# Optimization experiments

Hardware: AMD Instinct MI355X
Metric: run time of the kernel (lower is better)

Reference implementation:

```python
import jax, jax.numpy as jnp
import numpy as np

B, C, H, W = 4, 256, 64, 64
G = 32          # GroupNorm groups
EPS = 1e-6


def setup_inputs() -> dict:
    key = jax.random.key(0)
    ks = jax.random.split(key, 6)
    inp = {
        "x": jax.random.normal(ks[0], (B, C, H, W), dtype=jnp.float32),
        "gamma": jnp.ones((C,), jnp.float32),
        "beta": jnp.zeros((C,), jnp.float32),
        "wq": jax.random.normal(ks[1], (C, C), jnp.float32) * 0.02,
        "bq": jnp.zeros((C,), jnp.float32),
        "wk": jax.random.normal(ks[2], (C, C), jnp.float32) * 0.02,
        "bk": jnp.zeros((C,), jnp.float32),
        "wv": jax.random.normal(ks[3], (C, C), jnp.float32) * 0.02,
        "bv": jnp.zeros((C,), jnp.float32),
        "wp": jax.random.normal(ks[4], (C, C), jnp.float32) * 0.02,
        "bp": jnp.zeros((C,), jnp.float32),
    }
    return inp


def _group_norm(x, gamma, beta):
    b, c, h, w = x.shape
    xs = x.reshape(b, G, c // G, h, w)
    mu = xs.mean(axis=(2, 3, 4), keepdims=True)
    var = xs.var(axis=(2, 3, 4), keepdims=True)  # biased, matches torch GroupNorm
    xn = ((xs - mu) * jax.lax.rsqrt(var + EPS)).reshape(b, c, h, w)
    return xn * gamma[None, :, None, None] + beta[None, :, None, None]


def _conv1x1(s, w, bias):
    # 1x1 conv == per-pixel channel matmul
    return jnp.einsum('oc,bchw->bohw', w, s) + bias[None, :, None, None]


def reference(x, gamma, beta, wq, bq, wk, bk, wv, bv, wp, bp):
    b, c, h, w = x.shape
    s = _group_norm(x, gamma, beta)
    q = _conv1x1(s, wq, bq).reshape(b, c, h * w)  # [B, C, N]
    k = _conv1x1(s, wk, bk).reshape(b, c, h * w)
    v = _conv1x1(s, wv, bv).reshape(b, c, h * w)
    # scores[b,i,j] = sum_c q[b,c,i] k[b,c,j], scaled by C^-1/2
    scores = jnp.einsum('bci,bcj->bij', q, k) * (c ** -0.5)
    attn = jax.nn.softmax(scores, axis=2)
    # h_[b,c,i] = sum_j v[b,c,j] attn[b,i,j]
    h_ = jnp.einsum('bij,bcj->bci', attn, v).reshape(b, c, h, w)
    h_ = _conv1x1(h_, wp, bp)
    return x + h_
```

## Files before the change

### kernel.cpp

```cpp
#include <hip/hip_runtime.h>

#define BB 4
#define CCH 256
#define NPIX 4096
#define EPS 1e-6f

typedef __attribute__((ext_vector_type(8))) short bf16x8;
typedef __attribute__((ext_vector_type(4))) float f32x4;
typedef __attribute__((ext_vector_type(16))) float f32x16;

__device__ __forceinline__ unsigned short f2bf(float f) {
    return (unsigned short)((__float_as_uint(f) + 0x8000u) >> 16);
}
__device__ __forceinline__ float bf2f(unsigned short h) {
    return __uint_as_float((unsigned)h << 16);
}
__device__ __forceinline__ void gl2lds16(const void* g, void* l) {
    __builtin_amdgcn_global_load_lds(
        (const __attribute__((address_space(1))) unsigned int*)g,
        (__attribute__((address_space(3))) unsigned int*)l, 16, 0, 0);
}

__global__ __launch_bounds__(256) void gn_stats(
    const float* __restrict__ x, float2* __restrict__ pst,
    const float* __restrict__ wq, const float* __restrict__ wk,
    const float* __restrict__ wv, const float* __restrict__ wp,
    unsigned short* __restrict__ wb) {
    int bid = blockIdx.x;
    int t = threadIdx.x;
    if (bid >= 256) {
        int e = (bid - 256) * 256 + t;
        const float* srcs[4] = {wp, wq, wk, wv};
#pragma unroll
        for (int m = 0; m < 4; ++m) {
            float4 v = ((const float4*)srcs[m])[e];
            ushort4 hh;
            hh.x = f2bf(v.x); hh.y = f2bf(v.y);
            hh.z = f2bf(v.z); hh.w = f2bf(v.w);
            *(ushort4*)(wb + (size_t)m * 65536 + (size_t)e * 4) = hh;
        }
        return;
    }
    int b = bid >> 6, g = (bid >> 1) & 31, h = bid & 1;
    const float4* x4 = (const float4*)(x + (size_t)(b * CCH + g * 8) * NPIX);
    float s = 0.f, ss = 0.f;
    for (int e = h * 4096 + t; e < h * 4096 + 4096; e += 256) {
        float4 v = x4[e];
        s += v.x + v.y + v.z + v.w;
        ss += v.x * v.x + v.y * v.y + v.z * v.z + v.w * v.w;
    }
    __shared__ float rs[256], rss[256];
    rs[t] = s; rss[t] = ss;
    __syncthreads();
    for (int off = 128; off > 0; off >>= 1) {
        if (t < (unsigned)off) {
            rs[t] += rs[t + off];
            rss[t] += rss[t + off];
        }
        __syncthreads();
    }
    if (t == 0) pst[bid] = make_float2(rs[0], rss[0]);
}

__global__ __launch_bounds__(256) void gn_norm(
    const float* __restrict__ x, const float2* __restrict__ pst,
    const float* __restrict__ gamma, const float* __restrict__ beta,
    unsigned short* __restrict__ sb) {
    int bid = blockIdx.x;
    int b = bid >> 6, g = (bid >> 1) & 31, h = bid & 1;
    float2 p0 = pst[bid & ~1];
    float2 p1 = pst[bid | 1];
    const float inv = 1.0f / (float)(8 * NPIX);
    float m = (p0.x + p1.x) * inv;
    float var = (p0.y + p1.y) * inv - m * m;
    float rstd = rsqrtf(var + EPS);
    float scale[8], shift[8];
#pragma unroll
    for (int ci = 0; ci < 8; ++ci) {
        float ga = gamma[g * 8 + ci], be = beta[g * 8 + ci];
        scale[ci] = rstd * ga;
        shift[ci] = be - m * scale[ci];
    }
    const float4* x4 = (const float4*)(x + (size_t)(b * CCH + g * 8) * NPIX);
#pragma unroll 1
    for (int r = 0; r < 2; ++r) {
        int pq = h * 512 + r * 256 + threadIdx.x;
        __align__(16) unsigned short hh[4][8];
#pragma unroll
        for (int ci = 0; ci < 8; ++ci) {
            float4 v = x4[ci * 1024 + pq];
            hh[0][ci] = f2bf(v.x * scale[ci] + shift[ci]);
            hh[1][ci] = f2bf(v.y * scale[ci] + shift[ci]);
            hh[2][ci] = f2bf(v.z * scale[ci] + shift[ci]);
            hh[3][ci] = f2bf(v.w * scale[ci] + shift[ci]);
        }
        size_t base = ((size_t)(b * NPIX + pq * 4) << 8) + g * 8;
#pragma unroll
        for (int p = 0; p < 4; ++p)
            *(uint4*)(sb + base + (size_t)p * 256) = *(const uint4*)hh[p];
    }
}

__global__ __launch_bounds__(256) void qkv_mfma(
    const unsigned short* __restrict__ sb, const unsigned short* __restrict__ wb,
    const float* __restrict__ bq, const float* __restrict__ bk,
    const float* __restrict__ bv,
    unsigned short* __restrict__ qT, unsigned short* __restrict__ kT,
    unsigned short* __restrict__ vB) {
    __shared__ __align__(16) char lds[34816];
    const int tid = threadIdx.x, lane = tid & 63, w = tid >> 6;
    const int ln15 = lane & 15, q = lane >> 4;
    const int n0 = blockIdx.x * 128;
    const int co0 = blockIdx.y * 128;
    const int z = blockIdx.z;
    const unsigned short* wm = wb + (size_t)(z + 1) * 65536;
    const float* bias = (z == 0) ? bq : (z == 1) ? bk : bv;

    f32x4 acc[2][8];
#pragma unroll
    for (int i2 = 0; i2 < 2; ++i2)
#pragma unroll
        for (int nf = 0; nf < 8; ++nf) {
            acc[i2][nf][0] = 0.f; acc[i2][nf][1] = 0.f;
            acc[i2][nf][2] = 0.f; acc[i2][nf][3] = 0.f;
        }

#pragma unroll 1
    for (int kt = 0; kt < 4; ++kt) {
#pragma unroll
        for (int r = 0; r < 4; ++r) {
            int gch = r * 256 + tid;
            int row = gch >> 3, sidx = gch & 7;
            int cc = sidx ^ (row & 7);
            gl2lds16(sb + ((size_t)(n0 + row) << 8) + kt * 64 + cc * 8,
                     &lds[r * 4096 + w * 1024]);
            gl2lds16(wm + ((size_t)(co0 + row) << 8) + kt * 64 + cc * 8,
                     &lds[16384 + r * 4096 + w * 1024]);
        }
        __syncthreads();
#pragma unroll
        for (int kk = 0; kk < 2; ++kk) {
            int kc = kk * 4 + q;
            bf16x8 af[2], bf[8];
#pragma unroll
            for (int i2 = 0; i2 < 2; ++i2) {
                int row = w * 32 + i2 * 16 + ln15;
                af[i2] = *(const bf16x8*)&lds[row * 128 + ((kc ^ (row & 7)) << 4)];
            }
#pragma unroll
            for (int nf = 0; nf < 8; ++nf) {
                int row = nf * 16 + ln15;
                bf[nf] = *(const bf16x8*)&lds[16384 + row * 128 + ((kc ^ (row & 7)) << 4)];
            }
#pragma unroll
            for (int i2 = 0; i2 < 2; ++i2)
#pragma unroll
                for (int nf = 0; nf < 8; ++nf)
                    acc[i2][nf] = __builtin_amdgcn_mfma_f32_16x16x32_bf16(
                        af[i2], bf[nf], acc[i2][nf], 0, 0, 0);
        }
        __syncthreads();
    }

    float bias_l[8];
#pragma unroll
    for (int nf = 0; nf < 8; ++nf) bias_l[nf] = bias[co0 + nf * 16 + ln15];
    const float scl = (z == 0) ? 0.0625f : 1.0f;
    unsigned short* T = (unsigned short*)lds;
    if (z < 2) {
#pragma unroll
        for (int i2 = 0; i2 < 2; ++i2)
#pragma unroll
            for (int nf = 0; nf < 8; ++nf)
#pragma unroll
                for (int r = 0; r < 4; ++r) {
                    int n_l = w * 32 + i2 * 16 + q * 4 + r;
                    int co_l = nf * 16 + ln15;
                    T[n_l * 136 + co_l] = f2bf((acc[i2][nf][r] + bias_l[nf]) * scl);
                }
    } else {
#pragma unroll
        for (int i2 = 0; i2 < 2; ++i2)
#pragma unroll
            for (int nf = 0; nf < 8; ++nf)
#pragma unroll
                for (int r = 0; r < 4; ++r) {
                    int n_l = w * 32 + i2 * 16 + q * 4 + r;
                    int co_l = nf * 16 + ln15;
                    T[co_l * 136 + n_l] = f2bf(acc[i2][nf][r] + bias_l[nf]);
                }
    }
    __syncthreads();
    int row = tid >> 1, half = tid & 1;
    const uint4* src = (const uint4*)&T[row * 136 + half * 64];
    uint4* dst;
    if (z < 2) {
        unsigned short* qk = (z == 0) ? qT : kT;
        dst = (uint4*)(qk + ((size_t)(n0 + row) << 8) + co0 + half * 64);
    } else {
        int b2 = n0 >> 12, pix0 = n0 & 4095;
        dst = (uint4*)(vB + ((size_t)(b2 * CCH + co0 + row) << 12) + pix0 + half * 64);
    }
#pragma unroll
    for (int u = 0; u < 8; ++u) dst[u] = src[u];
}

__global__ __launch_bounds__(512, 1) void attn_mfma(
    const unsigned short* __restrict__ qT, const unsigned short* __restrict__ kT,
    const unsigned short* __restrict__ vB,
    unsigned short* __restrict__ pO, float* __restrict__ pml) {
    __shared__ __align__(16) char lds[147456];
    const int tid = threadIdx.x, lane = tid & 63, w = tid >> 6;
    const int l31 = lane & 31, lh = lane >> 5;
    const int bx = blockIdx.x;
    const int xk = bx & 7;
    const int b = xk >> 1, bjh = xk & 1;
    const int itile = bx >> 3;
    const int i0 = itile * 128;
    const int jbase = bjh * 2048;
    const size_t nb = (size_t)b * NPIX;
    const int iqb = (w >> 1) * 32;
    const int jh = w & 1, jwb = jh * 32;
    const int ipb = (w & 1) * 64;
    const int cqb = (w >> 1) * 64;

#pragma unroll
    for (int t = 0; t < 8; ++t) {
        int gch = (w * 8 + t) * 64 + lane;
        int row = gch >> 5, sc = gch & 31;
        int cc = sc ^ (row & 7);
        gl2lds16(qT + ((nb + i0 + row) << 8) + cc * 8, &lds[(w * 8 + t) * 1024]);
    }
    __syncthreads();
    bf16x8 qf[16];
    {
        int row = iqb + l31;
#pragma unroll
        for (int kc = 0; kc < 16; ++kc) {
            int sc = kc * 2 + lh;
            qf[kc] = *(const bf16x8*)&lds[row * 512 + ((sc ^ (row & 7)) << 4)];
        }
    }
    __syncthreads();

    f32x16 O[2][2];
#pragma unroll
    for (int ig = 0; ig < 2; ++ig)
#pragma unroll
        for (int cg = 0; cg < 2; ++cg)
#pragma unroll
            for (int r = 0; r < 16; ++r) O[ig][cg][r] = 0.f;
    float l_acc[16];
#pragma unroll
    for (int r = 0; r < 16; ++r) l_acc[r] = 0.f;

    {
        const int j0 = jbase;
#pragma unroll
        for (int t = 0; t < 4; ++t) {
            int gch = (w * 4 + t) * 64 + lane;
            int row = gch >> 5, sc = gch & 31;
            int cc = sc ^ (row & 7);
            gl2lds16(kT + ((nb + j0 + row) << 8) + cc * 8, &lds[(w * 4 + t) * 1024]);
        }
#pragma unroll
        for (int t = 0; t < 4; ++t) {
            int gch = (w * 4 + t) * 64 + lane;
            int c = gch >> 3, sv = gch & 7;
            int jc = sv ^ (c & 7);
            gl2lds16(vB + ((size_t)(b * CCH + c) << 12) + j0 + jc * 8,
                     &lds[65536 + (w * 4 + t) * 1024]);
        }
    }

#pragma unroll 1
    for (int jt = 0; jt < 32; ++jt) {
        const int kb_ = (jt & 1) * 32768;
        const int vb_ = 65536 + (jt & 1) * 32768;
        const int kbn = ((jt + 1) & 1) * 32768;
        const int vbn = 65536 + ((jt + 1) & 1) * 32768;

        asm volatile("s_waitcnt vmcnt(4)" ::: "memory");
        __builtin_amdgcn_s_barrier();

        f32x16 S0, S1;
#pragma unroll
        for (int r = 0; r < 16; ++r) { S0[r] = 0.f; S1[r] = 0.f; }
        __builtin_amdgcn_s_setprio(1);
        {
            int krow = jwb + l31;
            int ksw = kb_ + krow * 512;
#pragma unroll
            for (int kc = 0; kc < 8; ++kc) {
                int sc0 = (2 * kc) * 2 + lh;
                int sc1 = (2 * kc + 1) * 2 + lh;
                bf16x8 k0 = *(const bf16x8*)&lds[ksw + ((sc0 ^ (krow & 7)) << 4)];
                bf16x8 k1 = *(const bf16x8*)&lds[ksw + ((sc1 ^ (krow & 7)) << 4)];
                S0 = __builtin_amdgcn_mfma_f32_32x32x16_bf16(qf[2 * kc], k0, S0, 0, 0, 0);
                S1 = __builtin_amdgcn_mfma_f32_32x32x16_bf16(qf[2 * kc + 1], k1, S1, 0, 0, 0);
            }
        }
        __builtin_amdgcn_s_setprio(0);

        {
            int col = jwb + l31;
            int chs = (col >> 3) << 4;
            int cof = (col & 7) << 1;
#pragma unroll
            for (int r = 0; r < 16; ++r) {
                float p = __expf(S0[r] + S1[r]);
                l_acc[r] += p;
                int row = iqb + (r & 3) + 8 * (r >> 2) + 4 * lh;
                *(unsigned short*)&lds[131072 + row * 128 +
                    (chs ^ ((row & 7) << 4)) + cof] = f2bf(p);
            }
        }
        asm volatile("s_waitcnt lgkmcnt(0)" ::: "memory");
        __builtin_amdgcn_sched_barrier(0);
        asm volatile("s_waitcnt vmcnt(0)" ::: "memory");
        __builtin_amdgcn_s_barrier();

        if (jt < 31) {
            const int j0n = jbase + (jt + 1) * 64;
#pragma unroll
            for (int t = 0; t < 4; ++t) {
                int gch = (w * 4 + t) * 64 + lane;
                int row = gch >> 5, sc = gch & 31;
                int cc = sc ^ (row & 7);
                gl2lds16(kT + ((nb + j0n + row) << 8) + cc * 8,
                         &lds[kbn + (w * 4 + t) * 1024]);
            }
        }

        __builtin_amdgcn_s_setprio(1);
        {
            int pr0 = ipb + l31, pr1 = ipb + 32 + l31;
            int vc0 = cqb + l31, vc1 = cqb + 32 + l31;
#pragma unroll
            for (int kc = 0; kc < 4; ++kc) {
                int pc = kc * 2 + lh;
                bf16x8 pf0 = *(const bf16x8*)&lds[131072 + pr0 * 128 + ((pc ^ (pr0 & 7)) << 4)];
                bf16x8 pf1 = *(const bf16x8*)&lds[131072 + pr1 * 128 + ((pc ^ (pr1 & 7)) << 4)];
                bf16x8 vf0 = *(const bf16x8*)&lds[vb_ + vc0 * 128 + ((pc ^ (vc0 & 7)) << 4)];
                bf16x8 vf1 = *(const bf16x8*)&lds[vb_ + vc1 * 128 + ((pc ^ (vc1 & 7)) << 4)];
                O[0][0] = __builtin_amdgcn_mfma_f32_32x32x16_bf16(pf0, vf0, O[0][0], 0, 0, 0);
                O[0][1] = __builtin_amdgcn_mfma_f32_32x32x16_bf16(pf0, vf1, O[0][1], 0, 0, 0);
                O[1][0] = __builtin_amdgcn_mfma_f32_32x32x16_bf16(pf1, vf0, O[1][0], 0, 0, 0);
                O[1][1] = __builtin_amdgcn_mfma_f32_32x32x16_bf16(pf1, vf1, O[1][1], 0, 0, 0);
            }
        }
        __builtin_amdgcn_s_setprio(0);

        if (jt < 31) {
            const int j0n = jbase + (jt + 1) * 64;
#pragma unroll
            for (int t = 0; t < 4; ++t) {
                int gch = (w * 4 + t) * 64 + lane;
                int c = gch >> 3, sv = gch & 7;
                int jc = sv ^ (c & 7);
                gl2lds16(vB + ((size_t)(b * CCH + c) << 12) + j0n + jc * 8,
                         &lds[vbn + (w * 4 + t) * 1024]);
            }
        }
    }

    size_t pbase = (size_t)bx * (128 * 256);
#pragma unroll
    for (int ig = 0; ig < 2; ++ig)
#pragma unroll
        for (int cg = 0; cg < 2; ++cg)
#pragma unroll
            for (int r = 0; r < 16; ++r) {
                int i = ipb + ig * 32 + (r & 3) + 8 * (r >> 2) + 4 * lh;
                int c = cqb + cg * 32 + l31;
                pO[pbase + i * 256 + c] = f2bf(O[ig][cg][r]);
            }
#pragma unroll
    for (int r = 0; r < 16; ++r) {
        float l = l_acc[r];
        l += __shfl_xor(l, 1);
        l += __shfl_xor(l, 2);
        l += __shfl_xor(l, 4);
        l += __shfl_xor(l, 8);
        l += __shfl_xor(l, 16);
        if (l31 == 0) {
            int row = iqb + (r & 3) + 8 * (r >> 2) + 4 * lh;
            pml[bx * 256 + jh * 128 + row] = l;
        }
    }
}

__global__ __launch_bounds__(256) void attn_merge(
    const unsigned short* __restrict__ pO, const float* __restrict__ pml,
    unsigned short* __restrict__ hN) {
    int bid = blockIdx.x;
    int b = bid & 3, itile = (bid >> 2) & 31, ih = (bid >> 7) & 1;
    int base = itile * 8 + b * 2;
    __shared__ float fs[64];
    int t = threadIdx.x;
    if (t < 64) {
        float l = 0.f;
#pragma unroll
        for (int s = 0; s < 2; ++s) {
            int px = (base + s) * 256 + ih * 64 + t;
            l += pml[px] + pml[px + 128];
        }
        fs[t] = 1.0f / l;
    }
    __syncthreads();
    int i = t >> 2, cq = t & 3;
    float f = fs[i];
    int row = ih * 64 + i;
    size_t nrow = ((size_t)(b * NPIX + itile * 128 + row)) << 8;
#pragma unroll
    for (int p = 0; p < 16; ++p) {
        int c = p * 16 + cq * 4;
        float o0 = 0.f, o1 = 0.f, o2 = 0.f, o3 = 0.f;
#pragma unroll
        for (int s = 0; s < 2; ++s) {
            ushort4 a = *(const ushort4*)&pO[(size_t)(base + s) * 32768 + row * 256 + c];
            o0 += bf2f(a.x); o1 += bf2f(a.y); o2 += bf2f(a.z); o3 += bf2f(a.w);
        }
        ushort4 h;
        h.x = f2bf(o0 * f); h.y = f2bf(o1 * f);
        h.z = f2bf(o2 * f); h.w = f2bf(o3 * f);
        *(ushort4*)&hN[nrow + c] = h;
    }
}

__global__ __launch_bounds__(256) void proj_mfma(
    const unsigned short* __restrict__ hN, const unsigned short* __restrict__ wb,
    const float* __restrict__ bp, const float* __restrict__ x,
    float* __restrict__ out) {
    __shared__ __align__(16) char lds[34816];
    const int tid = threadIdx.x, lane = tid & 63, w = tid >> 6;
    const int ln15 = lane & 15, q = lane >> 4;
    const int n0 = blockIdx.x * 128;
    const int co0 = blockIdx.y * 128;

    f32x4 acc[2][8];
#pragma unroll
    for (int i2 = 0; i2 < 2; ++i2)
#pragma unroll
        for (int nf = 0; nf < 8; ++nf) {
            acc[i2][nf][0] = 0.f; acc[i2][nf][1] = 0.f;
            acc[i2][nf][2] = 0.f; acc[i2][nf][3] = 0.f;
        }

#pragma unroll 1
    for (int kt = 0; kt < 4; ++kt) {
#pragma unroll
        for (int r = 0; r < 4; ++r) {
            int gch = r * 256 + tid;
            int row = gch >> 3, sidx = gch & 7;
            int cc = sidx ^ (row & 7);
            gl2lds16(hN + ((size_t)(n0 + row) << 8) + kt * 64 + cc * 8,
                     &lds[r * 4096 + w * 1024]);
            gl2lds16(wb + ((size_t)(co0 + row) << 8) + kt * 64 + cc * 8,
                     &lds[16384 + r * 4096 + w * 1024]);
        }
        __syncthreads();
#pragma unroll
        for (int kk = 0; kk < 2; ++kk) {
            int kc = kk * 4 + q;
            bf16x8 af[2], bf[8];
#pragma unroll
            for (int i2 = 0; i2 < 2; ++i2) {
                int row = w * 32 + i2 * 16 + ln15;
                af[i2] = *(const bf16x8*)&lds[row * 128 + ((kc ^ (row & 7)) << 4)];
            }
#pragma unroll
            for (int nf = 0; nf < 8; ++nf) {
                int row = nf * 16 + ln15;
                bf[nf] = *(const bf16x8*)&lds[16384 + row * 128 + ((kc ^ (row & 7)) << 4)];
            }
#pragma unroll
            for (int i2 = 0; i2 < 2; ++i2)
#pragma unroll
                for (int nf = 0; nf < 8; ++nf)
                    acc[i2][nf] = __builtin_amdgcn_mfma_f32_16x16x32_bf16(
                        af[i2], bf[nf], acc[i2][nf], 0, 0, 0);
        }
        __syncthreads();
    }

    unsigned short* T = (unsigned short*)lds;
#pragma unroll
    for (int i2 = 0; i2 < 2; ++i2)
#pragma unroll
        for (int nf = 0; nf < 8; ++nf)
#pragma unroll
            for (int r = 0; r < 4; ++r) {
                int n_l = w * 32 + i2 * 16 + q * 4 + r;
                int co_l = nf * 16 + ln15;
                T[co_l * 136 + n_l] = f2bf(acc[i2][nf][r]);
            }
    __syncthreads();
    int row = tid >> 1, half = tid & 1;
    int b2 = n0 >> 12, pix0 = n0 & 4095;
    float br = bp[co0 + row];
    size_t gidx = (((size_t)(b2 * CCH + co0 + row)) << 12) + pix0 + half * 64;
    const unsigned short* trow = &T[row * 136 + half * 64];
#pragma unroll
    for (int u = 0; u < 16; ++u) {
        float4 xv = *(const float4*)&x[gidx + u * 4];
        ushort4 tv = *(const ushort4*)&trow[u * 4];
        float4 o;
        o.x = xv.x + br + bf2f(tv.x);
        o.y = xv.y + br + bf2f(tv.y);
        o.z = xv.z + br + bf2f(tv.z);
        o.w = xv.w + br + bf2f(tv.w);
        *(float4*)&out[gidx + u * 4] = o;
    }
}

extern "C" void kernel_launch(void* const* d_in, const int* in_sizes, int n_in,
                              void* d_out, int out_size, void* d_ws, size_t ws_size,
                              hipStream_t stream) {
    const float* x     = (const float*)d_in[0];
    const float* gamma = (const float*)d_in[1];
    const float* beta  = (const float*)d_in[2];
    const float* wq    = (const float*)d_in[3];
    const float* bq    = (const float*)d_in[4];
    const float* wk    = (const float*)d_in[5];
    const float* bk    = (const float*)d_in[6];
    const float* wv    = (const float*)d_in[7];
    const float* bv    = (const float*)d_in[8];
    const float* wp    = (const float*)d_in[9];
    const float* bp    = (const float*)d_in[10];
    float* out = (float*)d_out;

    char* p = (char*)d_ws;
    unsigned short* sb  = (unsigned short*)p; p += 8388608;
    unsigned short* hN  = sb;
    unsigned short* wb  = (unsigned short*)p; p += 524288;
    unsigned short* pO  = (unsigned short*)p; p += 16777216;
    float*          pml = (float*)p;          p += 262144;
    float2*         pst = (float2*)p;         p += 4096;
    unsigned short* qT  = (unsigned short*)p; p += 8388608;
    unsigned short* kT  = (unsigned short*)p; p += 8388608;
    unsigned short* vB  = (unsigned short*)p;

    gn_stats<<<320, 256, 0, stream>>>(x, pst, wq, wk, wv, wp, wb);
    gn_norm<<<256, 256, 0, stream>>>(x, pst, gamma, beta, sb);
    qkv_mfma<<<dim3(128, 2, 3), 256, 0, stream>>>(sb, wb, bq, bk, bv, qT, kT, vB);
    attn_mfma<<<256, 512, 0, stream>>>(qT, kT, vB, pO, pml);
    attn_merge<<<256, 256, 0, stream>>>(pO, pml, hN);
    proj_mfma<<<dim3(128, 2), 256, 0, stream>>>(hN, wb, bp, x, out);
}
```

Before: 215.4 us.

## Keep softmax probabilities in registers and compute transposed S for direct PV MFMA

```diff
diff --git a/kernel.cpp b/kernel.cpp
--- a/kernel.cpp
+++ b/kernel.cpp
@@ -19,6 +19,17 @@
     __builtin_amdgcn_global_load_lds(
         (const __attribute__((address_space(1))) unsigned int*)g,
         (__attribute__((address_space(3))) unsigned int*)l, 16, 0, 0);
+}
+__device__ __forceinline__ unsigned int cvtpk(float a, float b) {
+    unsigned int r;
+    asm("v_cvt_pk_bf16_f32 %0, %1, %2" : "=v"(r) : "v"(a), "v"(b));
+    return r;
+}
+__device__ __forceinline__ void plswap(unsigned int& a, unsigned int& b, bool hi) {
+    unsigned int pa_ = (unsigned int)__shfl_xor((int)a, 32);
+    unsigned int pb_ = (unsigned int)__shfl_xor((int)b, 32);
+    a = hi ? pb_ : a;
+    b = hi ? b : pa_;
 }
 
 __global__ __launch_bounds__(256) void gn_stats(
@@ -209,9 +220,10 @@
     const unsigned short* __restrict__ qT, const unsigned short* __restrict__ kT,
     const unsigned short* __restrict__ vB,
     unsigned short* __restrict__ pO, float* __restrict__ pml) {
-    __shared__ __align__(16) char lds[147456];
+    __shared__ __align__(16) char lds[131072];
     const int tid = threadIdx.x, lane = tid & 63, w = tid >> 6;
     const int l31 = lane & 31, lh = lane >> 5;
+    const bool hi = (lh != 0);
     const int bx = blockIdx.x;
     const int xk = bx & 7;
     const int b = xk >> 1, bjh = xk & 1;
@@ -221,8 +233,6 @@
     const size_t nb = (size_t)b * NPIX;
     const int iqb = (w >> 1) * 32;
     const int jh = w & 1, jwb = jh * 32;
-    const int ipb = (w & 1) * 64;
-    const int cqb = (w >> 1) * 64;
 
 #pragma unroll
     for (int t = 0; t < 8; ++t) {
@@ -243,16 +253,12 @@
     }
     __syncthreads();
 
-    f32x16 O[2][2];
-#pragma unroll
-    for (int ig = 0; ig < 2; ++ig)
-#pragma unroll
-        for (int cg = 0; cg < 2; ++cg)
-#pragma unroll
-            for (int r = 0; r < 16; ++r) O[ig][cg][r] = 0.f;
-    float l_acc[16];
-#pragma unroll
-    for (int r = 0; r < 16; ++r) l_acc[r] = 0.f;
+    f32x16 O[8];
+#pragma unroll
+    for (int ct = 0; ct < 8; ++ct)
+#pragma unroll
+        for (int r = 0; r < 16; ++r) O[ct][r] = 0.f;
+    float l_lane = 0.f;
 
     {
         const int j0 = jbase;
@@ -283,40 +289,42 @@
         asm volatile("s_waitcnt vmcnt(4)" ::: "memory");
         __builtin_amdgcn_s_barrier();
 
-        f32x16 S0, S1;
-#pragma unroll
-        for (int r = 0; r < 16; ++r) { S0[r] = 0.f; S1[r] = 0.f; }
+        f32x16 S;
+#pragma unroll
+        for (int r = 0; r < 16; ++r) S[r] = 0.f;
         __builtin_amdgcn_s_setprio(1);
         {
             int krow = jwb + l31;
             int ksw = kb_ + krow * 512;
-#pragma unroll
-            for (int kc = 0; kc < 8; ++kc) {
-                int sc0 = (2 * kc) * 2 + lh;
-                int sc1 = (2 * kc + 1) * 2 + lh;
-                bf16x8 k0 = *(const bf16x8*)&lds[ksw + ((sc0 ^ (krow & 7)) << 4)];
-                bf16x8 k1 = *(const bf16x8*)&lds[ksw + ((sc1 ^ (krow & 7)) << 4)];
-                S0 = __builtin_amdgcn_mfma_f32_32x32x16_bf16(qf[2 * kc], k0, S0, 0, 0, 0);
-                S1 = __builtin_amdgcn_mfma_f32_32x32x16_bf16(qf[2 * kc + 1], k1, S1, 0, 0, 0);
+            int kx = krow & 7;
+#pragma unroll
+            for (int kc = 0; kc < 16; ++kc) {
+                bf16x8 kf = *(const bf16x8*)&lds[ksw + (((kc * 2 + lh) ^ kx) << 4)];
+                S = __builtin_amdgcn_mfma_f32_32x32x16_bf16(kf, qf[kc], S, 0, 0, 0);
             }
         }
         __builtin_amdgcn_s_setprio(0);
 
+        float p[16];
+#pragma unroll
+        for (int r = 0; r < 16; ++r) p[r] = __expf(S[r]);
         {
-            int col = jwb + l31;
-            int chs = (col >> 3) << 4;
-            int cof = (col & 7) << 1;
-#pragma unroll
-            for (int r = 0; r < 16; ++r) {
-                float p = __expf(S0[r] + S1[r]);
-                l_acc[r] += p;
-                int row = iqb + (r & 3) + 8 * (r >> 2) + 4 * lh;
-                *(unsigned short*)&lds[131072 + row * 128 +
-                    (chs ^ ((row & 7) << 4)) + cof] = f2bf(p);
-            }
-        }
-        asm volatile("s_waitcnt lgkmcnt(0)" ::: "memory");
-        __builtin_amdgcn_sched_barrier(0);
+            float ls = 0.f;
+#pragma unroll
+            for (int r = 0; r < 16; ++r) ls += p[r];
+            l_lane += ls;
+        }
+        union { unsigned int u[4]; bf16x8 v; } c0, c1;
+        c0.u[0] = cvtpk(p[0], p[1]);  c0.u[1] = cvtpk(p[2], p[3]);
+        c0.u[2] = cvtpk(p[4], p[5]);  c0.u[3] = cvtpk(p[6], p[7]);
+        plswap(c0.u[0], c0.u[2], hi);
+        plswap(c0.u[1], c0.u[3], hi);
+        c1.u[0] = cvtpk(p[8], p[9]);  c1.u[1] = cvtpk(p[10], p[11]);
+        c1.u[2] = cvtpk(p[12], p[13]); c1.u[3] = cvtpk(p[14], p[15]);
+        plswap(c1.u[0], c1.u[2], hi);
+        plswap(c1.u[1], c1.u[3], hi);
+        bf16x8 pa0 = c0.v, pa1 = c1.v;
+
         asm volatile("s_waitcnt vmcnt(0)" ::: "memory");
         __builtin_amdgcn_s_barrier();
 
@@ -333,21 +341,15 @@
         }
 
         __builtin_amdgcn_s_setprio(1);
-        {
-            int pr0 = ipb + l31, pr1 = ipb + 32 + l31;
-            int vc0 = cqb + l31, vc1 = cqb + 32 + l31;
-#pragma unroll
-            for (int kc = 0; kc < 4; ++kc) {
-                int pc = kc * 2 + lh;
-                bf16x8 pf0 = *(const bf16x8*)&lds[131072 + pr0 * 128 + ((pc ^ (pr0 & 7)) << 4)];
-                bf16x8 pf1 = *(const bf16x8*)&lds[131072 + pr1 * 128 + ((pc ^ (pr1 & 7)) << 4)];
-                bf16x8 vf0 = *(const bf16x8*)&lds[vb_ + vc0 * 128 + ((pc ^ (vc0 & 7)) << 4)];
-                bf16x8 vf1 = *(const bf16x8*)&lds[vb_ + vc1 * 128 + ((pc ^ (vc1 & 7)) << 4)];
-                O[0][0] = __builtin_amdgcn_mfma_f32_32x32x16_bf16(pf0, vf0, O[0][0], 0, 0, 0);
-                O[0][1] = __builtin_amdgcn_mfma_f32_32x32x16_bf16(pf0, vf1, O[0][1], 0, 0, 0);
-                O[1][0] = __builtin_amdgcn_mfma_f32_32x32x16_bf16(pf1, vf0, O[1][0], 0, 0, 0);
-                O[1][1] = __builtin_amdgcn_mfma_f32_32x32x16_bf16(pf1, vf1, O[1][1], 0, 0, 0);
-            }
+#pragma unroll
+        for (int ct = 0; ct < 8; ++ct) {
+            int vrow = ct * 32 + l31;
+            int vbase = vb_ + vrow * 128;
+            int vx = vrow & 7;
+            bf16x8 vf0 = *(const bf16x8*)&lds[vbase + (((jh * 4 + lh) ^ vx) << 4)];
+            bf16x8 vf1 = *(const bf16x8*)&lds[vbase + (((jh * 4 + 2 + lh) ^ vx) << 4)];
+            O[ct] = __builtin_amdgcn_mfma_f32_32x32x16_bf16(pa0, vf0, O[ct], 0, 0, 0);
+            O[ct] = __builtin_amdgcn_mfma_f32_32x32x16_bf16(pa1, vf1, O[ct], 0, 0, 0);
         }
         __builtin_amdgcn_s_setprio(0);
 
@@ -364,30 +366,33 @@
         }
     }
 
+    __syncthreads();
+    float* xch = (float*)lds;
+    const int ib = w >> 1;
+    if (jh == 1) {
+#pragma unroll
+        for (int ct = 0; ct < 8; ++ct)
+#pragma unroll
+            for (int r = 0; r < 16; ++r) {
+                int il = (r & 3) + 8 * (r >> 2) + 4 * lh;
+                xch[ib * 8192 + il * 256 + ct * 32 + l31] = O[ct][r];
+            }
+    }
+    __syncthreads();
     size_t pbase = (size_t)bx * (128 * 256);
-#pragma unroll
-    for (int ig = 0; ig < 2; ++ig)
-#pragma unroll
-        for (int cg = 0; cg < 2; ++cg)
+    if (jh == 0) {
+#pragma unroll
+        for (int ct = 0; ct < 8; ++ct)
 #pragma unroll
             for (int r = 0; r < 16; ++r) {
-                int i = ipb + ig * 32 + (r & 3) + 8 * (r >> 2) + 4 * lh;
-                int c = cqb + cg * 32 + l31;
-                pO[pbase + i * 256 + c] = f2bf(O[ig][cg][r]);
-            }
-#pragma unroll
-    for (int r = 0; r < 16; ++r) {
-        float l = l_acc[r];
-        l += __shfl_xor(l, 1);
-        l += __shfl_xor(l, 2);
-        l += __shfl_xor(l, 4);
-        l += __shfl_xor(l, 8);
-        l += __shfl_xor(l, 16);
-        if (l31 == 0) {
-            int row = iqb + (r & 3) + 8 * (r >> 2) + 4 * lh;
-            pml[bx * 256 + jh * 128 + row] = l;
-        }
-    }
+                int il = (r & 3) + 8 * (r >> 2) + 4 * lh;
+                float o = O[ct][r] + xch[ib * 8192 + il * 256 + ct * 32 + l31];
+                pO[pbase + (size_t)(iqb + il) * 256 + ct * 32 + l31] = f2bf(o);
+            }
+    }
+    l_lane += __shfl_xor(l_lane, 32);
+    if (lane < 32)
+        pml[bx * 256 + jh * 128 + iqb + lane] = l_lane;
 }
 
 __global__ __launch_bounds__(256) void attn_merge(
```

New measurement: 256.7 us. +19.2%, slower.

## Fuse GroupNorm stats with normalization and fold attention merge into projection

Applied to the files above, without the earlier changes.

```diff
diff --git a/kernel.cpp b/kernel.cpp
--- a/kernel.cpp
+++ b/kernel.cpp
@@ -20,16 +20,24 @@
         (const __attribute__((address_space(1))) unsigned int*)g,
         (__attribute__((address_space(3))) unsigned int*)l, 16, 0, 0);
 }
-
-__global__ __launch_bounds__(256) void gn_stats(
-    const float* __restrict__ x, float2* __restrict__ pst,
+__device__ __forceinline__ unsigned int comb2(unsigned int u0, unsigned int u1,
+                                              float f) {
+    float lo = (bf2f((unsigned short)u0) + bf2f((unsigned short)u1)) * f;
+    float hi = (bf2f((unsigned short)(u0 >> 16)) +
+                bf2f((unsigned short)(u1 >> 16))) * f;
+    return (unsigned int)f2bf(lo) | ((unsigned int)f2bf(hi) << 16);
+}
+
+__global__ __launch_bounds__(512) void gn_fused(
+    const float* __restrict__ x, const float* __restrict__ gamma,
+    const float* __restrict__ beta,
     const float* __restrict__ wq, const float* __restrict__ wk,
     const float* __restrict__ wv, const float* __restrict__ wp,
-    unsigned short* __restrict__ wb) {
+    unsigned short* __restrict__ sb, unsigned short* __restrict__ wb) {
     int bid = blockIdx.x;
     int t = threadIdx.x;
-    if (bid >= 256) {
-        int e = (bid - 256) * 256 + t;
+    if (bid >= 128) {
+        int e = (bid - 128) * 512 + t;
         const float* srcs[4] = {wp, wq, wk, wv};
 #pragma unroll
         for (int m = 0; m < 4; ++m) {
@@ -41,38 +49,29 @@
         }
         return;
     }
-    int b = bid >> 6, g = (bid >> 1) & 31, h = bid & 1;
+    int b = bid >> 5, g = bid & 31;
     const float4* x4 = (const float4*)(x + (size_t)(b * CCH + g * 8) * NPIX);
     float s = 0.f, ss = 0.f;
-    for (int e = h * 4096 + t; e < h * 4096 + 4096; e += 256) {
+    for (int e = t; e < 8192; e += 512) {
         float4 v = x4[e];
         s += v.x + v.y + v.z + v.w;
         ss += v.x * v.x + v.y * v.y + v.z * v.z + v.w * v.w;
     }
-    __shared__ float rs[256], rss[256];
-    rs[t] = s; rss[t] = ss;
+#pragma unroll
+    for (int off = 1; off < 64; off <<= 1) {
+        s += __shfl_xor(s, off);
+        ss += __shfl_xor(ss, off);
+    }
+    __shared__ float ws[8], wss[8];
+    int w = t >> 6, lane = t & 63;
+    if (lane == 0) { ws[w] = s; wss[w] = ss; }
     __syncthreads();
-    for (int off = 128; off > 0; off >>= 1) {
-        if (t < (unsigned)off) {
-            rs[t] += rs[t + off];
-            rss[t] += rss[t + off];
-        }
-        __syncthreads();
-    }
-    if (t == 0) pst[bid] = make_float2(rs[0], rss[0]);
-}
-
-__global__ __launch_bounds__(256) void gn_norm(
-    const float* __restrict__ x, const float2* __restrict__ pst,
-    const float* __restrict__ gamma, const float* __restrict__ beta,
-    unsigned short* __restrict__ sb) {
-    int bid = blockIdx.x;
-    int b = bid >> 6, g = (bid >> 1) & 31, h = bid & 1;
-    float2 p0 = pst[bid & ~1];
-    float2 p1 = pst[bid | 1];
+    float S = 0.f, SS = 0.f;
+#pragma unroll
+    for (int i = 0; i < 8; ++i) { S += ws[i]; SS += wss[i]; }
     const float inv = 1.0f / (float)(8 * NPIX);
-    float m = (p0.x + p1.x) * inv;
-    float var = (p0.y + p1.y) * inv - m * m;
+    float m = S * inv;
+    float var = SS * inv - m * m;
     float rstd = rsqrtf(var + EPS);
     float scale[8], shift[8];
 #pragma unroll
@@ -81,10 +80,9 @@
         scale[ci] = rstd * ga;
         shift[ci] = be - m * scale[ci];
     }
-    const float4* x4 = (const float4*)(x + (size_t)(b * CCH + g * 8) * NPIX);
 #pragma unroll 1
     for (int r = 0; r < 2; ++r) {
-        int pq = h * 512 + r * 256 + threadIdx.x;
+        int pq = r * 512 + t;
         __align__(16) unsigned short hh[4][8];
 #pragma unroll
         for (int ci = 0; ci < 8; ++ci) {
@@ -390,54 +388,26 @@
     }
 }
 
-__global__ __launch_bounds__(256) void attn_merge(
+__global__ __launch_bounds__(256) void proj_mfma(
     const unsigned short* __restrict__ pO, const float* __restrict__ pml,
-    unsigned short* __restrict__ hN) {
-    int bid = blockIdx.x;
-    int b = bid & 3, itile = (bid >> 2) & 31, ih = (bid >> 7) & 1;
-    int base = itile * 8 + b * 2;
-    __shared__ float fs[64];
-    int t = threadIdx.x;
-    if (t < 64) {
-        float l = 0.f;
-#pragma unroll
-        for (int s = 0; s < 2; ++s) {
-            int px = (base + s) * 256 + ih * 64 + t;
-            l += pml[px] + pml[px + 128];
-        }
-        fs[t] = 1.0f / l;
-    }
-    __syncthreads();
-    int i = t >> 2, cq = t & 3;
-    float f = fs[i];
-    int row = ih * 64 + i;
-    size_t nrow = ((size_t)(b * NPIX + itile * 128 + row)) << 8;
-#pragma unroll
-    for (int p = 0; p < 16; ++p) {
-        int c = p * 16 + cq * 4;
-        float o0 = 0.f, o1 = 0.f, o2 = 0.f, o3 = 0.f;
-#pragma unroll
-        for (int s = 0; s < 2; ++s) {
-            ushort4 a = *(const ushort4*)&pO[(size_t)(base + s) * 32768 + row * 256 + c];
-            o0 += bf2f(a.x); o1 += bf2f(a.y); o2 += bf2f(a.z); o3 += bf2f(a.w);
-        }
-        ushort4 h;
-        h.x = f2bf(o0 * f); h.y = f2bf(o1 * f);
-        h.z = f2bf(o2 * f); h.w = f2bf(o3 * f);
-        *(ushort4*)&hN[nrow + c] = h;
-    }
-}
-
-__global__ __launch_bounds__(256) void proj_mfma(
-    const unsigned short* __restrict__ hN, const unsigned short* __restrict__ wb,
-    const float* __restrict__ bp, const float* __restrict__ x,
-    float* __restrict__ out) {
-    __shared__ __align__(16) char lds[34816];
+    const unsigned short* __restrict__ wb, const float* __restrict__ bp,
+    const float* __restrict__ x, float* __restrict__ out) {
+    __shared__ __align__(16) char lds[35328];
+    float* fs = (float*)&lds[34816];
     const int tid = threadIdx.x, lane = tid & 63, w = tid >> 6;
     const int ln15 = lane & 15, q = lane >> 4;
     const int n0 = blockIdx.x * 128;
     const int co0 = blockIdx.y * 128;
 
+    if (tid < 128) {
+        int n = n0 + tid;
+        int bb = n >> 12, pix = n & 4095, it = pix >> 7, ii = pix & 127;
+        int base = (it * 8 + bb * 2) * 256 + ii;
+        float l = pml[base] + pml[base + 128] + pml[base + 256] + pml[base + 384];
+        fs[tid] = 1.0f / l;
+    }
+    __syncthreads();
+
     f32x4 acc[2][8];
 #pragma unroll
     for (int i2 = 0; i2 < 2; ++i2)
@@ -454,10 +424,27 @@
             int gch = r * 256 + tid;
             int row = gch >> 3, sidx = gch & 7;
             int cc = sidx ^ (row & 7);
-            gl2lds16(hN + ((size_t)(n0 + row) << 8) + kt * 64 + cc * 8,
-                     &lds[r * 4096 + w * 1024]);
             gl2lds16(wb + ((size_t)(co0 + row) << 8) + kt * 64 + cc * 8,
                      &lds[16384 + r * 4096 + w * 1024]);
+        }
+#pragma unroll
+        for (int r = 0; r < 4; ++r) {
+            int gch = r * 256 + tid;
+            int row = gch >> 3, sidx = gch & 7;
+            int cc = sidx ^ (row & 7);
+            int c = kt * 64 + cc * 8;
+            int n = n0 + row;
+            int bb = n >> 12, pix = n & 4095, it = pix >> 7, ii = pix & 127;
+            size_t pb = (size_t)(it * 8 + bb * 2) * 32768 + (size_t)ii * 256 + c;
+            uint4 a0 = *(const uint4*)&pO[pb];
+            uint4 a1 = *(const uint4*)&pO[pb + 32768];
+            float f = fs[row];
+            uint4 o;
+            o.x = comb2(a0.x, a1.x, f);
+            o.y = comb2(a0.y, a1.y, f);
+            o.z = comb2(a0.z, a1.z, f);
+            o.w = comb2(a0.w, a1.w, f);
+            *(uint4*)&lds[r * 4096 + w * 1024 + lane * 16] = o;
         }
         __syncthreads();
 #pragma unroll
@@ -532,19 +519,15 @@
 
     char* p = (char*)d_ws;
     unsigned short* sb  = (unsigned short*)p; p += 8388608;
-    unsigned short* hN  = sb;
     unsigned short* wb  = (unsigned short*)p; p += 524288;
     unsigned short* pO  = (unsigned short*)p; p += 16777216;
     float*          pml = (float*)p;          p += 262144;
-    float2*         pst = (float2*)p;         p += 4096;
     unsigned short* qT  = (unsigned short*)p; p += 8388608;
     unsigned short* kT  = (unsigned short*)p; p += 8388608;
     unsigned short* vB  = (unsigned short*)p;
 
-    gn_stats<<<320, 256, 0, stream>>>(x, pst, wq, wk, wv, wp, wb);
-    gn_norm<<<256, 256, 0, stream>>>(x, pst, gamma, beta, sb);
+    gn_fused<<<160, 512, 0, stream>>>(x, gamma, beta, wq, wk, wv, wp, sb, wb);
     qkv_mfma<<<dim3(128, 2, 3), 256, 0, stream>>>(sb, wb, bq, bk, bv, qT, kT, vB);
     attn_mfma<<<256, 512, 0, stream>>>(qT, kT, vB, pO, pml);
-    attn_merge<<<256, 256, 0, stream>>>(pO, pml, hN);
-    proj_mfma<<<dim3(128, 2), 256, 0, stream>>>(hN, wb, bp, x, out);
-}
+    proj_mfma<<<dim3(128, 2), 256, 0, stream>>>(pO, pml, wb, bp, x, out);
+}
```

Measured after the change: 209.8 us, median of 2. -2.6%, faster.
